# Optimization experiments

Measured on AMD Instinct MI355X. Metric: run time of the kernel, lower is better.

Reference implementation:

```python
import jax, jax.numpy as jnp
import numpy as np
from jax import lax

M_ROWS, N_COLS = 2048, 4096
ADMM_ITERS = 30
CG_ITERS = 15


def setup_inputs() -> dict:
    key = jax.random.key(0)
    ks = jax.random.split(key, 6)
    A = jax.random.normal(ks[0], (M_ROWS, N_COLS), dtype=jnp.float32) / np.sqrt(N_COLS)
    c = jax.random.normal(ks[1], (N_COLS, 1), dtype=jnp.float32)
    # finite box bounds with lb < ub (isinf mask path in the original is vacuous here)
    lb = -(jnp.abs(jax.random.normal(ks[2], (M_ROWS, 1), dtype=jnp.float32)) + 0.1)
    ub = jnp.abs(jax.random.normal(ks[3], (M_ROWS, 1), dtype=jnp.float32)) + 0.1
    # positive diagonal scalings from the LP preconditioning (Ruiz-style)
    d = 0.5 + jax.random.uniform(ks[4], (N_COLS, 1), dtype=jnp.float32)
    e = 0.5 + jax.random.uniform(ks[5], (M_ROWS, 1), dtype=jnp.float32)
    return {
        "A": A, "c": c, "lb": lb, "ub": ub, "d": d, "e": e,
        "gamma_c": jnp.ones((1,), jnp.float32),   # gamma_c_mul * gamma_c
        "gamma_b": jnp.ones((1,), jnp.float32),   # gamma_b_mul * gamma_b
        "rho": jnp.ones((1,), jnp.float32),
        "sigma": jnp.full((1,), 1e-6, jnp.float32),  # exp(sigma_log), sigma_log=log(1e-6)
        "alpha": jnp.full((1,), 1.6, jnp.float32),
    }


def _pcg(matvec, b, Minv, x0, iters):
    """Fixed-iteration preconditioned conjugate gradient for SPD matvec."""
    r0 = b - matvec(x0)
    z0 = Minv(r0)
    rz0 = jnp.vdot(r0, z0)

    def body(carry, _):
        x, r, p, rz = carry
        Kp = matvec(p)
        a = rz / jnp.vdot(p, Kp)
        x = x + a * p
        r = r - a * Kp
        zv = Minv(r)
        rz_new = jnp.vdot(r, zv)
        p = zv + (rz_new / rz) * p
        return (x, r, p, rz_new), None

    (x, _, _, _), _ = lax.scan(body, (x0, r0, z0, rz0), None, length=iters)
    return x


def _admm_lp(A, c, lb, ub, d, e, gamma_c, gamma_b, rho, sigma, alpha):
    gc, gb = gamma_c[0], gamma_b[0]
    rho_s, sig_s, al_s = rho[0], sigma[0], alpha[0]
    m, n = A.shape

    c_s = gc * (d * c)                 # (n,1) scaled cost
    lb_s = gb * e * lb                 # (m,1)
    ub_s = gb * e * ub                 # (m,1)

    # diagonal preconditioner M = sigma + rho * ||A_:,j||^2
    Acnorm2 = jnp.sum(A * A, axis=0)[:, None]      # (n,1)
    Mdiag = sig_s + rho_s * Acnorm2
    Minv = lambda v: v / Mdiag
    Kop = lambda v: rho_s * (A.T @ (A @ v)) + sig_s * v

    x0 = jnp.zeros((n, 1), A.dtype)
    z0 = jnp.zeros((m, 1), A.dtype)
    y0 = jnp.zeros((m, 1), A.dtype)
    xt0 = jnp.zeros((n, 1), A.dtype)

    def step(carry, _):
        x, z, y, xtilde = carry
        right = sig_s * x - c_s + A.T @ (rho_s * z - y)
        xtilde = _pcg(Kop, right, Minv, xtilde, CG_ITERS)
        ztilde = A @ xtilde
        x = al_s * xtilde + (1.0 - al_s) * x
        ztilde = al_s * ztilde + (1.0 - al_s) * z
        z = jnp.clip(ztilde + y / rho_s, lb_s, ub_s)
        y = y + rho_s * (ztilde - z)
        return (x, z, y, xtilde), None

    (x, z, y, xtilde), _ = lax.scan(step, (x0, z0, y0, xt0), None, length=ADMM_ITERS)
    return x * d / gb                   # unscaled LP solution (n,1)


def reference(A, c, lb, ub, d, e, gamma_c, gamma_b, rho, sigma, alpha):
    return _admm_lp(A, c, lb, ub, d, e, gamma_c, gamma_b, rho, sigma, alpha)
```

## Files before the change

kernel.cpp:

```cpp
#include <hip/hip_runtime.h>

#define NWG 256
#define NT  512
#define ROWS 8
#define JPT 8
#define CPW 16
#define RPT 64
#define NDIM 4096
#define MROWS 2048
#define N_ADMM 30
#define N_CG 15

typedef unsigned long long ull;
typedef float f32x4 __attribute__((ext_vector_type(4)));

static_assert(NWG * ROWS == MROWS, "row partition");
static_assert(NT * JPT == NDIM, "col partition");
static_assert(NWG * CPW == NDIM, "col-slice partition");
static_assert(32 * RPT == MROWS, "col-slice rows");

__device__ __forceinline__ float wred64(float v) {
#pragma unroll
  for (int m = 32; m > 0; m >>= 1) v += __shfl_xor(v, m, 64);
  return v;
}
__device__ __forceinline__ float sum8(float v) {
  v += __shfl_xor(v, 1, 64); v += __shfl_xor(v, 2, 64); v += __shfl_xor(v, 4, 64);
  return v;
}
__device__ __forceinline__ float sum16(float v) {
  v += __shfl_xor(v, 1, 64); v += __shfl_xor(v, 2, 64);
  v += __shfl_xor(v, 4, 64); v += __shfl_xor(v, 8, 64);
  return v;
}
__device__ __forceinline__ void st64(ull* p, ull v) {
  __hip_atomic_store(p, v, __ATOMIC_RELAXED, __HIP_MEMORY_SCOPE_AGENT);
}
__device__ __forceinline__ ull ld64(const ull* p) {
  return __hip_atomic_load(p, __ATOMIC_RELAXED, __HIP_MEMORY_SCOPE_AGENT);
}
__device__ __forceinline__ f32x4 ntf4(const float* p) {
  return __builtin_nontemporal_load((const f32x4*)p);
}
__device__ __forceinline__ ull pk2(float a, float b) {
  return ((ull)__float_as_uint(b) << 32) | (ull)__float_as_uint(a);
}

#define WS_KILL   128
#define WS_BANK0  8192
#define WS_BANK1  24576
#define WS_Z      49152
#define WS_XT     65536
#define WS_T      81920
#define WS_U      90112

__global__ __launch_bounds__(NT, 2)
void admm_lp_kernel(const float* __restrict__ A, const float* __restrict__ cvec,
                    const float* __restrict__ lbv, const float* __restrict__ ubv,
                    const float* __restrict__ dvec, const float* __restrict__ evec,
                    const float* __restrict__ gcp, const float* __restrict__ gbp,
                    const float* __restrict__ rhop, const float* __restrict__ sigp,
                    const float* __restrict__ alp,
                    float* __restrict__ out, unsigned char* __restrict__ ws)
{
  const int tid = threadIdx.x;
  const int w = blockIdx.x;
  const int wv = tid >> 6;
  const int lane = tid & 63;
  const int j0 = tid * JPT;
  const int row0 = w * ROWS;
  const int g = tid >> 4;
  const int l = tid & 15;

  unsigned* kill = (unsigned*)(ws + WS_KILL);
  ull* fbank[2] = { (ull*)(ws + WS_BANK0), (ull*)(ws + WS_BANK1) };
  float* z_g  = (float*)(ws + WS_Z);
  float* xt_g = (float*)(ws + WS_XT);
  float* t_g  = (float*)(ws + WS_T);
  float* u_g  = (float*)(ws + WS_U);
  ull* z64 = (ull*)z_g; ull* xt64 = (ull*)xt_g; ull* t64 = (ull*)t_g; ull* u64 = (ull*)u_g;

  __shared__ float s_scal[6];
  __shared__ float dred[8][ROWS];
  __shared__ float sredA[32][16];
  __shared__ float sredB[32][16];
  __shared__ int s_dead;

  float areg[ROWS][JPT];
  float acol[RPT];

  unsigned gen = 0;

  auto wait_prod = [&](unsigned G) {
    if (s_dead) return;
    ull* fp = &fbank[G & 1][(size_t)(wv * 32 + (lane & 31)) * 8];
    int spin = 0;
    for (;;) {
      ull v = ld64(fp);
      if (__all((unsigned)(v >> 32) >= G)) break;
      __builtin_amdgcn_s_sleep(1);
      if ((++spin & 127) == 0) {
        if (__hip_atomic_load(kill, __ATOMIC_RELAXED, __HIP_MEMORY_SCOPE_AGENT) != 0u ||
            spin > 300000) {
          s_dead = 1;
          __hip_atomic_store(kill, 1u, __ATOMIC_RELAXED, __HIP_MEMORY_SCOPE_AGENT);
          break;
        }
      }
    }
    asm volatile("" ::: "memory");
    __builtin_amdgcn_sched_barrier(0);
  };

  auto poll_all = [&](unsigned G) -> float {
    ull v0 = 0, v1 = 0, v2 = 0, v3 = 0;
    if (!s_dead) {
      ull* fb = fbank[G & 1];
      ull* f0 = &fb[(size_t)(lane * 4 + 0) * 8];
      ull* f1 = &fb[(size_t)(lane * 4 + 1) * 8];
      ull* f2 = &fb[(size_t)(lane * 4 + 2) * 8];
      ull* f3 = &fb[(size_t)(lane * 4 + 3) * 8];
      int spin = 0;
      for (;;) {
        v0 = ld64(f0); v1 = ld64(f1); v2 = ld64(f2); v3 = ld64(f3);
        bool ok = ((unsigned)(v0 >> 32) >= G) && ((unsigned)(v1 >> 32) >= G) &&
                  ((unsigned)(v2 >> 32) >= G) && ((unsigned)(v3 >> 32) >= G);
        if (__all(ok)) break;
        __builtin_amdgcn_s_sleep(1);
        if ((++spin & 127) == 0) {
          if (__hip_atomic_load(kill, __ATOMIC_RELAXED, __HIP_MEMORY_SCOPE_AGENT) != 0u ||
              spin > 300000) {
            s_dead = 1;
            __hip_atomic_store(kill, 1u, __ATOMIC_RELAXED, __HIP_MEMORY_SCOPE_AGENT);
            break;
          }
        }
      }
    }
    asm volatile("" ::: "memory");
    __builtin_amdgcn_sched_barrier(0);
    float s = __uint_as_float((unsigned)(v0 & 0xffffffffu))
            + __uint_as_float((unsigned)(v1 & 0xffffffffu))
            + __uint_as_float((unsigned)(v2 & 0xffffffffu))
            + __uint_as_float((unsigned)(v3 & 0xffffffffu));
    return wred64(s);
  };

  auto publish = [&](float partial) {
    asm volatile("s_waitcnt vmcnt(0)" ::: "memory");
    __builtin_amdgcn_sched_barrier(0);
    if (lane == 0 && !s_dead)
      st64(&fbank[(gen + 1) & 1][(size_t)w * 8],
           ((ull)(gen + 1) << 32) | (ull)__float_as_uint(partial));
  };

  if (tid == 0) {
    s_scal[0] = sigp[0]; s_scal[1] = rhop[0]; s_scal[2] = alp[0];
    s_scal[3] = gcp[0];  s_scal[4] = gbp[0];
    s_dead = 0;
  }
  {
#pragma unroll
    for (int r = 0; r < ROWS; ++r) {
      const float* ap = A + (size_t)(row0 + r) * NDIM + j0;
      const float4 a0 = *(const float4*)(ap);
      const float4 a1 = *(const float4*)(ap + 4);
      areg[r][0] = a0.x; areg[r][1] = a0.y; areg[r][2] = a0.z; areg[r][3] = a0.w;
      areg[r][4] = a1.x; areg[r][5] = a1.y; areg[r][6] = a1.z; areg[r][7] = a1.w;
    }
    float cn = 0.f;
#pragma unroll
    for (int r = 0; r < RPT; ++r) {
      acol[r] = A[(size_t)(g * RPT + r) * NDIM + w * CPW + l];
      cn += acol[r] * acol[r];
    }
    sredA[g][l] = cn;
  }
  __syncthreads();

  const float sig = s_scal[0], rho = s_scal[1], al = s_scal[2];

  float f_cs = 0.f, f_Md = 1.f, f_rl = 0.f, f_pch = 0.f, f_xtl = 0.f, f_xa = 0.f;
  float f_zown = 0.f, f_trow = 0.f, f_zb = 0.f, f_yb = 0.f, f_lbs = 0.f, f_ubs = 0.f;
  float rz_cur = 1.f, gbv = 1.f;

  if (wv == 0) {
    gbv = s_scal[4];
    if (lane < 8) {
      const float ee = evec[row0 + lane];
      f_lbs = gbv * ee * lbv[row0 + lane];
      f_ubs = gbv * ee * ubv[row0 + lane];
    }
    if (lane < 16) {
      f_cs = s_scal[3] * dvec[w * 16 + lane] * cvec[w * 16 + lane];
      float S = 0.f;
#pragma unroll
      for (int q = 0; q < 32; ++q) S += sredA[q][lane];
      f_Md = sig + rho * S;
      f_rl = -f_cs;
      f_zown = f_rl / f_Md;
    }
    float rzp = (lane < 16) ? f_rl * f_zown : 0.f;
    rzp = sum16(rzp);
    float a0 = __shfl(f_zown, (lane & 7) * 2, 64);
    float b0 = __shfl(f_zown, (lane & 7) * 2 + 1, 64);
    if (lane < 8) st64(&z64[(size_t)w * 8 + lane], pk2(a0, b0));
    publish(rzp);
  }
  ++gen;

  for (int admm = 0; admm < N_ADMM; ++admm) {
    for (int cg = 0; cg < N_CG; ++cg) {
      {
        wait_prod(gen);
        const f32x4 za = ntf4(z_g + j0);
        const f32x4 zc = ntf4(z_g + j0 + 4);
        const float zl[JPT] = {za.x, za.y, za.z, za.w, zc.x, zc.y, zc.z, zc.w};
        float dp[ROWS];
#pragma unroll
        for (int r = 0; r < ROWS; ++r) {
          float s = 0.f;
#pragma unroll
          for (int k = 0; k < JPT; ++k) s += areg[r][k] * zl[k];
          dp[r] = s;
        }
#pragma unroll
        for (int r = 0; r < ROWS; ++r) {
          const float t = wred64(dp[r]);
          if (lane == 0) dred[wv][r] = t;
        }
        __syncthreads();
        if (wv == 0) {
          const float rz_new = poll_all(gen);
          const float beta = (cg == 0) ? 0.f : rz_new / rz_cur;
          rz_cur = rz_new;
          float az = 0.f;
          if (lane < 8) {
#pragma unroll
            for (int q = 0; q < 8; ++q) az += dred[q][lane];
          }
          f_trow = az + beta * f_trow;
          f_pch  = f_zown + beta * f_pch;
          float st2 = (lane < 8) ? f_trow * f_trow : 0.f;
          st2 = sum8(st2);
          float sp2 = (lane < 16) ? f_pch * f_pch : 0.f;
          sp2 = sum16(sp2);
          const float part = rho * st2 + sig * sp2;
          float a0 = __shfl(f_trow, (lane & 3) * 2, 64);
          float b0 = __shfl(f_trow, (lane & 3) * 2 + 1, 64);
          if (lane < 4) st64(&t64[(size_t)w * 4 + lane], pk2(a0, b0));
          publish(part);
        }
        ++gen;
      }
      {
        wait_prod(gen);
        float up = 0.f;
#pragma unroll
        for (int r4 = 0; r4 < RPT / 4; ++r4) {
          const f32x4 tv = ntf4(t_g + g * RPT + r4 * 4);
          up += tv.x * acol[r4 * 4 + 0] + tv.y * acol[r4 * 4 + 1]
              + tv.z * acol[r4 * 4 + 2] + tv.w * acol[r4 * 4 + 3];
        }
        sredA[g][l] = up;
        __syncthreads();
        if (wv == 0) {
          const float pkp = poll_all(gen);
          const float alpha = rz_cur / pkp;
          float S = 0.f;
          if (lane < 16) {
#pragma unroll
            for (int q = 0; q < 32; ++q) S += sredA[q][lane];
          }
          const float Kp = rho * S + sig * f_pch;
          const float rn = f_rl - alpha * Kp;
          f_rl = rn;
          f_xtl += alpha * f_pch;
          f_zown = rn / f_Md;
          float rzp = (lane < 16) ? rn * f_zown : 0.f;
          rzp = sum16(rzp);
          float a0 = __shfl(f_zown, (lane & 7) * 2, 64);
          float b0 = __shfl(f_zown, (lane & 7) * 2 + 1, 64);
          if (lane < 8) st64(&z64[(size_t)w * 8 + lane], pk2(a0, b0));
          if (cg == N_CG - 1) {
            float c0 = __shfl(f_xtl, (lane & 7) * 2, 64);
            float d0 = __shfl(f_xtl, (lane & 7) * 2 + 1, 64);
            if (lane < 8) st64(&xt64[(size_t)w * 8 + lane], pk2(c0, d0));
          }
          publish(rzp);
        }
        ++gen;
      }
    }
    if (admm < N_ADMM - 1) {
      {
        wait_prod(gen);
        const f32x4 xv0 = ntf4(xt_g + j0);
        const f32x4 xv1 = ntf4(xt_g + j0 + 4);
        const float xl[JPT] = {xv0.x, xv0.y, xv0.z, xv0.w, xv1.x, xv1.y, xv1.z, xv1.w};
        float dp[ROWS];
#pragma unroll
        for (int r = 0; r < ROWS; ++r) {
          float s = 0.f;
#pragma unroll
          for (int k = 0; k < JPT; ++k) s += areg[r][k] * xl[k];
          dp[r] = s;
        }
#pragma unroll
        for (int r = 0; r < ROWS; ++r) {
          const float t = wred64(dp[r]);
          if (lane == 0) dred[wv][r] = t;
        }
        __syncthreads();
        if (wv == 0) {
          (void)poll_all(gen);
          float ztr = 0.f, urow = 0.f;
          if (lane < 8) {
#pragma unroll
            for (int q = 0; q < 8; ++q) ztr += dred[q][lane];
            const float zt = al * ztr + (1.f - al) * f_zb;
            float zn = fminf(fmaxf(zt + f_yb / rho, f_lbs), f_ubs);
            const float yn = f_yb + rho * (zt - zn);
            f_zb = zn; f_yb = yn;
            urow = rho * zn - yn;
          }
          f_xa = al * f_xtl + (1.f - al) * f_xa;
          float ta = __shfl(ztr,  (lane & 3) * 2, 64);
          float tb = __shfl(ztr,  (lane & 3) * 2 + 1, 64);
          float ua = __shfl(urow, (lane & 3) * 2, 64);
          float ub = __shfl(urow, (lane & 3) * 2 + 1, 64);
          if (lane < 4) {
            st64(&t64[(size_t)w * 4 + lane], pk2(ta, tb));
            st64(&u64[(size_t)w * 4 + lane], pk2(ua, ub));
          }
          publish(0.f);
        }
        ++gen;
      }
      {
        wait_prod(gen);
        float pk = 0.f, pr = 0.f;
#pragma unroll
        for (int r4 = 0; r4 < RPT / 4; ++r4) {
          const f32x4 tv = ntf4(t_g + g * RPT + r4 * 4);
          const f32x4 uv = ntf4(u_g + g * RPT + r4 * 4);
          pk += tv.x * acol[r4 * 4 + 0] + tv.y * acol[r4 * 4 + 1]
              + tv.z * acol[r4 * 4 + 2] + tv.w * acol[r4 * 4 + 3];
          pr += uv.x * acol[r4 * 4 + 0] + uv.y * acol[r4 * 4 + 1]
              + uv.z * acol[r4 * 4 + 2] + uv.w * acol[r4 * 4 + 3];
        }
        sredA[g][l] = pk; sredB[g][l] = pr;
        __syncthreads();
        if (wv == 0) {
          (void)poll_all(gen);
          float SK = 0.f, SR = 0.f;
          if (lane < 16) {
#pragma unroll
            for (int q = 0; q < 32; ++q) { SK += sredA[q][lane]; SR += sredB[q][lane]; }
          }
          const float right = sig * f_xa - f_cs + SR;
          const float Kx = rho * SK + sig * f_xtl;
          const float r0 = right - Kx;
          f_rl = r0;
          f_zown = r0 / f_Md;
          float rzp = (lane < 16) ? r0 * f_zown : 0.f;
          rzp = sum16(rzp);
          float a0 = __shfl(f_zown, (lane & 7) * 2, 64);
          float b0 = __shfl(f_zown, (lane & 7) * 2 + 1, 64);
          if (lane < 8) st64(&z64[(size_t)w * 8 + lane], pk2(a0, b0));
          publish(rzp);
        }
        ++gen;
      }
    }
  }
  if (wv == 0 && lane < 16) {
    const float xf = al * f_xtl + (1.f - al) * f_xa;
    out[w * 16 + lane] = xf * dvec[w * 16 + lane] / gbv;
  }
}

extern "C" void kernel_launch(void* const* d_in, const int* in_sizes, int n_in,
                              void* d_out, int out_size, void* d_ws, size_t ws_size,
                              hipStream_t stream) {
  const float* A   = (const float*)d_in[0];
  const float* c   = (const float*)d_in[1];
  const float* lb  = (const float*)d_in[2];
  const float* ub  = (const float*)d_in[3];
  const float* dv  = (const float*)d_in[4];
  const float* ev  = (const float*)d_in[5];
  const float* gc  = (const float*)d_in[6];
  const float* gb  = (const float*)d_in[7];
  const float* rho = (const float*)d_in[8];
  const float* sg  = (const float*)d_in[9];
  const float* al  = (const float*)d_in[10];
  float* out = (float*)d_out;
  unsigned char* ws = (unsigned char*)d_ws;

  (void)hipMemsetAsync(d_ws, 0, 40960, stream);

  admm_lp_kernel<<<dim3(NWG), dim3(NT), 0, stream>>>(
      A, c, lb, ub, dv, ev, gc, gb, rho, sg, al, out, ws);
}
```

Baseline: 5.776 ms.

## Replace flat all-to-all flag polling with two-level hierarchical barrier and reduction

Workgroups 0-7 each have one wave gather the 32 producer flags and partial sums of a group, reduce them, and publish a level-1 flag and partial. Every other wave and workgroup polls only the 8 level-1 slots, both for the barrier gate and for the global scalar reduction. This is meant to cut the number of flag cache lines each wave spins on and reduce contention in L2. In exchange the chain gains an extra hop of latency through the aggregator workgroups. The summation order of the reductions also changes.

```diff
diff --git a/kernel.cpp b/kernel.cpp
--- a/kernel.cpp
+++ b/kernel.cpp
@@ -49,6 +49,8 @@
 #define WS_KILL   128
 #define WS_BANK0  8192
 #define WS_BANK1  24576
+#define WS_L1B0   40960
+#define WS_L1B1   43008
 #define WS_Z      49152
 #define WS_XT     65536
 #define WS_T      81920
@@ -73,7 +75,8 @@
   const int l = tid & 15;
 
   unsigned* kill = (unsigned*)(ws + WS_KILL);
-  ull* fbank[2] = { (ull*)(ws + WS_BANK0), (ull*)(ws + WS_BANK1) };
+  ull* fbank[2]  = { (ull*)(ws + WS_BANK0), (ull*)(ws + WS_BANK1) };
+  ull* l1bank[2] = { (ull*)(ws + WS_L1B0),  (ull*)(ws + WS_L1B1)  };
   float* z_g  = (float*)(ws + WS_Z);
   float* xt_g = (float*)(ws + WS_XT);
   float* t_g  = (float*)(ws + WS_T);
@@ -91,41 +94,17 @@
 
   unsigned gen = 0;
 
-  auto wait_prod = [&](unsigned G) {
+  auto gate = [&](unsigned G) {
     if (s_dead) return;
-    ull* fp = &fbank[G & 1][(size_t)(wv * 32 + (lane & 31)) * 8];
-    int spin = 0;
-    for (;;) {
-      ull v = ld64(fp);
-      if (__all((unsigned)(v >> 32) >= G)) break;
-      __builtin_amdgcn_s_sleep(1);
-      if ((++spin & 127) == 0) {
-        if (__hip_atomic_load(kill, __ATOMIC_RELAXED, __HIP_MEMORY_SCOPE_AGENT) != 0u ||
-            spin > 300000) {
-          s_dead = 1;
-          __hip_atomic_store(kill, 1u, __ATOMIC_RELAXED, __HIP_MEMORY_SCOPE_AGENT);
-          break;
-        }
-      }
-    }
-    asm volatile("" ::: "memory");
-    __builtin_amdgcn_sched_barrier(0);
-  };
-
-  auto poll_all = [&](unsigned G) -> float {
-    ull v0 = 0, v1 = 0, v2 = 0, v3 = 0;
-    if (!s_dead) {
-      ull* fb = fbank[G & 1];
-      ull* f0 = &fb[(size_t)(lane * 4 + 0) * 8];
-      ull* f1 = &fb[(size_t)(lane * 4 + 1) * 8];
-      ull* f2 = &fb[(size_t)(lane * 4 + 2) * 8];
-      ull* f3 = &fb[(size_t)(lane * 4 + 3) * 8];
+    ull* l0 = fbank[G & 1];
+    ull* l1 = l1bank[G & 1];
+    if (w < 8 && wv == w) {
+      ull* fp = &l0[(size_t)(wv * 32 + (lane & 31)) * 8];
+      ull v;
       int spin = 0;
       for (;;) {
-        v0 = ld64(f0); v1 = ld64(f1); v2 = ld64(f2); v3 = ld64(f3);
-        bool ok = ((unsigned)(v0 >> 32) >= G) && ((unsigned)(v1 >> 32) >= G) &&
-                  ((unsigned)(v2 >> 32) >= G) && ((unsigned)(v3 >> 32) >= G);
-        if (__all(ok)) break;
+        v = ld64(fp);
+        if (__all((unsigned)(v >> 32) >= G)) break;
         __builtin_amdgcn_s_sleep(1);
         if ((++spin & 127) == 0) {
           if (__hip_atomic_load(kill, __ATOMIC_RELAXED, __HIP_MEMORY_SCOPE_AGENT) != 0u ||
@@ -136,14 +115,54 @@
           }
         }
       }
+      float pv = (lane < 32) ? __uint_as_float((unsigned)(v & 0xffffffffu)) : 0.f;
+      float s = wred64(pv);
+      if (lane == 0 && !s_dead)
+        st64(&l1[(size_t)wv * 8], ((ull)G << 32) | (ull)__float_as_uint(s));
+    } else {
+      ull* fp = &l1[(size_t)wv * 8];
+      int spin = 0;
+      for (;;) {
+        ull v = ld64(fp);
+        if (__all((unsigned)(v >> 32) >= G)) break;
+        __builtin_amdgcn_s_sleep(1);
+        if ((++spin & 127) == 0) {
+          if (__hip_atomic_load(kill, __ATOMIC_RELAXED, __HIP_MEMORY_SCOPE_AGENT) != 0u ||
+              spin > 300000) {
+            s_dead = 1;
+            __hip_atomic_store(kill, 1u, __ATOMIC_RELAXED, __HIP_MEMORY_SCOPE_AGENT);
+            break;
+          }
+        }
+      }
     }
     asm volatile("" ::: "memory");
     __builtin_amdgcn_sched_barrier(0);
-    float s = __uint_as_float((unsigned)(v0 & 0xffffffffu))
-            + __uint_as_float((unsigned)(v1 & 0xffffffffu))
-            + __uint_as_float((unsigned)(v2 & 0xffffffffu))
-            + __uint_as_float((unsigned)(v3 & 0xffffffffu));
-    return wred64(s);
+  };
+
+  auto global_sum = [&](unsigned G) -> float {
+    ull v = 0;
+    if (!s_dead) {
+      ull* fp = &l1bank[G & 1][(size_t)(lane & 7) * 8];
+      int spin = 0;
+      for (;;) {
+        v = ld64(fp);
+        if (__all((unsigned)(v >> 32) >= G)) break;
+        __builtin_amdgcn_s_sleep(1);
+        if ((++spin & 127) == 0) {
+          if (__hip_atomic_load(kill, __ATOMIC_RELAXED, __HIP_MEMORY_SCOPE_AGENT) != 0u ||
+              spin > 300000) {
+            s_dead = 1;
+            __hip_atomic_store(kill, 1u, __ATOMIC_RELAXED, __HIP_MEMORY_SCOPE_AGENT);
+            break;
+          }
+        }
+      }
+    }
+    asm volatile("" ::: "memory");
+    __builtin_amdgcn_sched_barrier(0);
+    float pv = (lane < 8) ? __uint_as_float((unsigned)(v & 0xffffffffu)) : 0.f;
+    return wred64(pv);
   };
 
   auto publish = [&](float partial) {
@@ -212,7 +231,7 @@
   for (int admm = 0; admm < N_ADMM; ++admm) {
     for (int cg = 0; cg < N_CG; ++cg) {
       {
-        wait_prod(gen);
+        gate(gen);
         const f32x4 za = ntf4(z_g + j0);
         const f32x4 zc = ntf4(z_g + j0 + 4);
         const float zl[JPT] = {za.x, za.y, za.z, za.w, zc.x, zc.y, zc.z, zc.w};
@@ -231,7 +250,7 @@
         }
         __syncthreads();
         if (wv == 0) {
-          const float rz_new = poll_all(gen);
+          const float rz_new = global_sum(gen);
           const float beta = (cg == 0) ? 0.f : rz_new / rz_cur;
           rz_cur = rz_new;
           float az = 0.f;
@@ -254,7 +273,7 @@
         ++gen;
       }
       {
-        wait_prod(gen);
+        gate(gen);
         float up = 0.f;
 #pragma unroll
         for (int r4 = 0; r4 < RPT / 4; ++r4) {
@@ -265,7 +284,7 @@
         sredA[g][l] = up;
         __syncthreads();
         if (wv == 0) {
-          const float pkp = poll_all(gen);
+          const float pkp = global_sum(gen);
           const float alpha = rz_cur / pkp;
           float S = 0.f;
           if (lane < 16) {
@@ -294,7 +313,7 @@
     }
     if (admm < N_ADMM - 1) {
       {
-        wait_prod(gen);
+        gate(gen);
         const f32x4 xv0 = ntf4(xt_g + j0);
         const f32x4 xv1 = ntf4(xt_g + j0 + 4);
         const float xl[JPT] = {xv0.x, xv0.y, xv0.z, xv0.w, xv1.x, xv1.y, xv1.z, xv1.w};
@@ -313,7 +332,7 @@
         }
         __syncthreads();
         if (wv == 0) {
-          (void)poll_all(gen);
+          (void)global_sum(gen);
           float ztr = 0.f, urow = 0.f;
           if (lane < 8) {
 #pragma unroll
@@ -338,7 +357,7 @@
         ++gen;
       }
       {
-        wait_prod(gen);
+        gate(gen);
         float pk = 0.f, pr = 0.f;
 #pragma unroll
         for (int r4 = 0; r4 < RPT / 4; ++r4) {
@@ -352,7 +371,7 @@
         sredA[g][l] = pk; sredB[g][l] = pr;
         __syncthreads();
         if (wv == 0) {
-          (void)poll_all(gen);
+          (void)global_sum(gen);
           float SK = 0.f, SR = 0.f;
           if (lane < 16) {
 #pragma unroll
@@ -397,7 +416,7 @@
   float* out = (float*)d_out;
   unsigned char* ws = (unsigned char*)d_ws;
 
-  (void)hipMemsetAsync(d_ws, 0, 40960, stream);
+  (void)hipMemsetAsync(d_ws, 0, 49152, stream);
 
   admm_lp_kernel<<<dim3(NWG), dim3(NT), 0, stream>>>(
       A, c, lb, ub, dv, ev, gc, gb, rho, sg, al, out, ws);
```

Measured after the change: 5.515 ms. 1.05x faster.
